# Kernel optimization log

Measured on AMD Instinct MI355X. Metric: run time of the kernel, lower is better.

## Reference

```python
import jax, jax.numpy as jnp
import numpy as np

BN_EPS = 1e-5


def setup_inputs() -> dict:
    key = jax.random.key(0)
    k1, k2, k3 = jax.random.split(key, 3)
    N, C_IN, C_OUT, K = 200000, 32, 64, 27
    data_in = jax.random.normal(k1, (1, C_IN, N, 1), dtype=jnp.float32)
    # Octree neighbor table: for each octant, indices of its 27 (3x3x3) neighbors.
    # ocnn uses -1 for empty neighbors; indices here are all valid, but the
    # reference still masks negatives for faithfulness.
    neigh = jax.random.randint(k2, (N, K), 0, N, dtype=jnp.int64)
    weight = jax.random.normal(k3, (C_OUT, C_IN, K), dtype=jnp.float32) * 0.05
    bn_gamma = jnp.ones((C_OUT,), dtype=jnp.float32)
    bn_beta = jnp.zeros((C_OUT,), dtype=jnp.float32)
    return {"data_in": data_in, "neigh": neigh, "weight": weight,
            "bn_gamma": bn_gamma, "bn_beta": bn_beta}


def reference(data_in, neigh, weight, bn_gamma, bn_beta):
    # data_in: [1, C_in, N, 1] (ocnn octree feature layout)
    x = data_in[0, :, :, 0]                      # [C_in, N]
    valid = neigh >= 0                           # [N, 27]
    idx = jnp.where(valid, neigh, 0)
    # octree2col: gather 27 neighbor features per octant -> [C_in, N, 27]
    col = x[:, idx] * valid[None, :, :].astype(x.dtype)
    # grouped GEMM: weight [C_out, C_in, 27] contracted with col
    out = jnp.einsum('ock,cnk->on', weight, col)  # [C_out, N]
    # BatchNorm2d in training mode: batch stats over the node axis, biased var
    mean = jnp.mean(out, axis=1, keepdims=True)
    var = jnp.mean(jnp.square(out - mean), axis=1, keepdims=True)
    out = (out - mean) * jax.lax.rsqrt(var + BN_EPS)
    out = out * bn_gamma[:, None] + bn_beta[:, None]
    out = jax.nn.relu(out)
    return out[None, :, :, None]                 # [1, C_out, N, 1]
```

## Files before the change

kernel.cpp:

```cpp
#include <hip/hip_runtime.h>

#define N_PTS 200000
#define C_IN  32
#define C_OUT 64
#define K_NB  27
#define BN_EPS 1e-5f
#define CBLK  3125

using bf16x8 = __attribute__((ext_vector_type(8))) short;
using f32x4  = __attribute__((ext_vector_type(4))) float;

typedef const __attribute__((address_space(1))) char GP;
typedef __attribute__((address_space(3))) char LP;

#define M_WT_OFF  0
#define M_AB_OFF  114688
#define M_PS_OFF  131072
#define M_XT_OFF  2097152
#define M_RAW_OFF 14897216
#define M_WS_NEED_B ((size_t)M_XT_OFF + (size_t)(N_PTS + 1) * C_IN * 2)
#define M_WS_NEED_A ((size_t)M_RAW_OFF + (size_t)C_OUT * N_PTS * 2)

#define F_WTK_OFF 0
#define F_AB_OFF  221184
#define F_PS_OFF  221824

__device__ __forceinline__ unsigned short f2bf(float f) {
    unsigned int u = __float_as_uint(f);
    u = (u + 0x7fffu + ((u >> 16) & 1u)) >> 16;
    return (unsigned short)u;
}
__device__ __forceinline__ unsigned short f2h(float f) {
    _Float16 h = (_Float16)f;
    unsigned short u; __builtin_memcpy(&u, &h, 2); return u;
}
__device__ __forceinline__ float h2f(unsigned short u) {
    _Float16 h; __builtin_memcpy(&h, &u, 2); return (float)h;
}

__global__ void k_prep(const float* __restrict__ x, const float* __restrict__ w,
                       unsigned short* __restrict__ xt, unsigned short* __restrict__ wt) {
    if (blockIdx.x < 782) {
        int n = blockIdx.x * 256 + threadIdx.x;
        if (n > N_PTS) return;
        unsigned short row[C_IN];
        if (n == N_PTS) {
#pragma unroll
            for (int c = 0; c < C_IN; ++c) row[c] = 0;
        } else {
#pragma unroll
            for (int c = 0; c < C_IN; ++c) row[c] = f2bf(x[(long long)c * N_PTS + n]);
        }
        uint4* dst = (uint4*)(xt + (long long)n * C_IN);
#pragma unroll
        for (int q = 0; q < 4; ++q) dst[q] = ((const uint4*)row)[q];
    } else {
        int i = (blockIdx.x - 782) * 256 + threadIdx.x;
        if (i >= 28 * C_OUT * C_IN) return;
        int c = i & 31, o = (i >> 5) & 63, k = i >> 11;
        wt[i] = (k < K_NB) ? f2bf(w[(o * C_IN + c) * K_NB + k]) : (unsigned short)0;
    }
}

template <int RAW16>
__launch_bounds__(256, 5)
__global__ void k_conv_mfma(const unsigned short* __restrict__ xt,
                            const int* __restrict__ neigh,
                            const unsigned short* __restrict__ wt,
                            float* __restrict__ out,
                            unsigned short* __restrict__ raw16,
                            float* __restrict__ ps) {
    __shared__ __align__(16) char lds_raw[6 * 4096 + K_NB * 64 * 4];
    char* bufB = lds_raw;
    int*  ntb  = (int*)(lds_raw + 24576);

    const int lane = threadIdx.x & 63;
    const int w    = threadIdx.x >> 6;
    const int l15  = lane & 15, lq = lane >> 4;
    const int n0   = blockIdx.x * 64;

    {
        int p  = threadIdx.x & 63;
        int kb = (threadIdx.x >> 6) * 7;
        const int* nrow = neigh + (long long)(n0 + p) * K_NB;
#pragma unroll
        for (int i = 0; i < 7; ++i) {
            int kk = kb + i;
            if (kk < K_NB) {
                int t = nrow[kk];
                ntb[kk * 64 + p] = ((unsigned)t < N_PTS) ? t : N_PTS;
            }
        }
    }
    __syncthreads();

    const char* xtb = (const char*)xt;
    const unsigned short* wtA = wt + w * 512 + l15 * 32 + lq * 8;
    const unsigned qoff = (unsigned)(lq * 16);

    unsigned bufB_a = (unsigned)(unsigned long long)(LP*)lds_raw;
    unsigned ntb_a  = bufB_a + 24576;
    unsigned badr   = bufB_a + (unsigned)(lq * 256 + l15 * 16);
    unsigned tadr   = ntb_a + (unsigned)(w * 64 + l15 * 4);

    f32x4 acc0 = {0.f,0.f,0.f,0.f}, acc1 = {0.f,0.f,0.f,0.f},
          acc2 = {0.f,0.f,0.f,0.f}, acc3 = {0.f,0.f,0.f,0.f};
    bf16x8 Ar[4];
    int tcur;

#define PSTEP(KK) \
    asm volatile("ds_read_b32 %0, %1 offset:%2" : "=v"(tcur) : "v"(tadr), "i"((KK)*256)); \
    asm volatile("s_waitcnt lgkmcnt(0)" ::: "memory"); \
    __builtin_amdgcn_sched_barrier(0); \
    __builtin_amdgcn_global_load_lds((GP*)(xtb + (unsigned long long)(unsigned)tcur * 64ull + qoff), \
        (LP*)(bufB + (KK)*4096 + w*1024), 16, 0, 0); \
    asm volatile("global_load_dwordx4 %0, %1, off" : "=v"(Ar[(KK)&3]) : "v"(wtA + (KK)*2048)); \
    __builtin_amdgcn_sched_barrier(0);

    PSTEP(0) PSTEP(1) PSTEP(2) PSTEP(3)
#undef PSTEP
    asm volatile("ds_read_b32 %0, %1 offset:%2" : "=v"(tcur) : "v"(tadr), "i"(4*256));

#define STEP(K, VM, PF, NT, LG) { \
    if (PF) { \
        asm volatile("s_waitcnt lgkmcnt(0)" ::: "memory"); \
        __builtin_amdgcn_sched_barrier(0); \
        __builtin_amdgcn_global_load_lds((GP*)(xtb + (unsigned long long)(unsigned)tcur * 64ull + qoff), \
            (LP*)(bufB + (((K)+4)%6)*4096 + w*1024), 16, 0, 0); \
    } \
    __builtin_amdgcn_sched_barrier(0); \
    asm volatile("s_waitcnt vmcnt(%0)" :: "i"(VM) : "memory"); \
    __builtin_amdgcn_sched_barrier(0); \
    asm volatile("s_barrier" ::: "memory"); \
    __builtin_amdgcn_sched_barrier(0); \
    bf16x8 b0, b1, b2, b3; \
    asm volatile("ds_read_b128 %0, %1 offset:%2" : "=v"(b0) : "v"(badr), "i"(((K)%6)*4096 + 0)); \
    asm volatile("ds_read_b128 %0, %1 offset:%2" : "=v"(b1) : "v"(badr), "i"(((K)%6)*4096 + 1024)); \
    asm volatile("ds_read_b128 %0, %1 offset:%2" : "=v"(b2) : "v"(badr), "i"(((K)%6)*4096 + 2048)); \
    asm volatile("ds_read_b128 %0, %1 offset:%2" : "=v"(b3) : "v"(badr), "i"(((K)%6)*4096 + 3072)); \
    if (NT) { asm volatile("ds_read_b32 %0, %1 offset:%2" : "=v"(tcur) : "v"(tadr), "i"(((K)+5)*256)); } \
    asm volatile("s_waitcnt lgkmcnt(%0)" :: "i"(LG) : "memory"); \
    __builtin_amdgcn_sched_barrier(0); \
    acc0 = __builtin_amdgcn_mfma_f32_16x16x32_bf16(Ar[(K)&3], b0, acc0, 0, 0, 0); \
    acc1 = __builtin_amdgcn_mfma_f32_16x16x32_bf16(Ar[(K)&3], b1, acc1, 0, 0, 0); \
    acc2 = __builtin_amdgcn_mfma_f32_16x16x32_bf16(Ar[(K)&3], b2, acc2, 0, 0, 0); \
    acc3 = __builtin_amdgcn_mfma_f32_16x16x32_bf16(Ar[(K)&3], b3, acc3, 0, 0, 0); \
    if (PF) { \
        asm volatile("global_load_dwordx4 %0, %1, off" : "=v"(Ar[((K)+4)&3]) : "v"(wtA + ((K)+4)*2048)); \
    } \
    __builtin_amdgcn_sched_barrier(0); \
}

    STEP(0,7,1,1,1)  STEP(1,7,1,1,1)  STEP(2,7,1,1,1)  STEP(3,7,1,1,1)
    STEP(4,7,1,1,1)  STEP(5,7,1,1,1)  STEP(6,7,1,1,1)  STEP(7,7,1,1,1)
    STEP(8,7,1,1,1)  STEP(9,7,1,1,1)  STEP(10,7,1,1,1) STEP(11,7,1,1,1)
    STEP(12,7,1,1,1) STEP(13,7,1,1,1) STEP(14,7,1,1,1) STEP(15,7,1,1,1)
    STEP(16,7,1,1,1) STEP(17,7,1,1,1) STEP(18,7,1,1,1) STEP(19,7,1,1,1)
    STEP(20,7,1,1,1) STEP(21,7,1,1,1) STEP(22,7,1,0,0)
    STEP(23,6,0,0,0) STEP(24,4,0,0,0) STEP(25,2,0,0,0) STEP(26,0,0,0,0)
#undef STEP

    asm volatile("s_waitcnt vmcnt(0) lgkmcnt(0)" ::: "memory");
    __builtin_amdgcn_sched_barrier(0);

    if (RAW16) {
#pragma unroll
        for (int r = 0; r < 4; ++r) {
            unsigned short* o = raw16 + (long long)(16 * w + lq * 4 + r) * N_PTS + n0 + l15;
            o[0]  = f2h(acc0[r]);
            o[16] = f2h(acc1[r]);
            o[32] = f2h(acc2[r]);
            o[48] = f2h(acc3[r]);
        }
    } else {
#pragma unroll
        for (int r = 0; r < 4; ++r) {
            float* o = out + (long long)(16 * w + lq * 4 + r) * N_PTS + n0 + l15;
            o[0]  = acc0[r];
            o[16] = acc1[r];
            o[32] = acc2[r];
            o[48] = acc3[r];
        }
    }

    f32x4 s  = acc0 + acc1 + acc2 + acc3;
    f32x4 sq = acc0 * acc0 + acc1 * acc1 + acc2 * acc2 + acc3 * acc3;
#pragma unroll
    for (int d = 1; d < 16; d <<= 1) {
#pragma unroll
        for (int r = 0; r < 4; ++r) {
            s[r]  += __shfl_xor(s[r], d);
            sq[r] += __shfl_xor(sq[r], d);
        }
    }
    if (l15 == 0) {
#pragma unroll
        for (int r = 0; r < 4; ++r) {
            int ch = 16 * w + lq * 4 + r;
            ps[blockIdx.x * 128 + ch]      = s[r];
            ps[blockIdx.x * 128 + 64 + ch] = sq[r];
        }
    }
}

__global__ void k_stats2(const float* __restrict__ ps, const float* __restrict__ gamma,
                         const float* __restrict__ beta, float* __restrict__ ab) {
    int ch = blockIdx.x;
    float s = 0.f, s2 = 0.f;
    for (int b = threadIdx.x; b < CBLK; b += 256) {
        s  += ps[b * 128 + ch];
        s2 += ps[b * 128 + 64 + ch];
    }
#pragma unroll
    for (int off = 32; off > 0; off >>= 1) {
        s  += __shfl_down(s, off, 64);
        s2 += __shfl_down(s2, off, 64);
    }
    __shared__ float r0[4], r1[4];
    int wv = threadIdx.x >> 6;
    if ((threadIdx.x & 63) == 0) { r0[wv] = s; r1[wv] = s2; }
    __syncthreads();
    if (threadIdx.x == 0) {
        float S  = r0[0] + r0[1] + r0[2] + r0[3];
        float S2 = r1[0] + r1[1] + r1[2] + r1[3];
        float mean = S / (float)N_PTS;
        float var  = S2 / (float)N_PTS - mean * mean;
        float a = gamma[ch] * rsqrtf(var + BN_EPS);
        float b = beta[ch] - mean * a;
        ab[ch]      = a;
        ab[64 + ch] = b;
    }
}

__global__ void k_norm16(const unsigned short* __restrict__ raw16, float* __restrict__ out,
                         const float* __restrict__ ab) {
    int i = blockIdx.x * 256 + threadIdx.x;
    const int tot8 = (C_OUT * N_PTS) / 8;
    if (i >= tot8) return;
    int o = (int)(((long long)i * 8) / N_PTS);
    float a = ab[o], b = ab[64 + o];
    union { uint4 u4; unsigned short us[8]; } U;
    U.u4 = ((const uint4*)raw16)[i];
    float4 r0, r1;
    r0.x = fmaxf(fmaf(h2f(U.us[0]), a, b), 0.f);
    r0.y = fmaxf(fmaf(h2f(U.us[1]), a, b), 0.f);
    r0.z = fmaxf(fmaf(h2f(U.us[2]), a, b), 0.f);
    r0.w = fmaxf(fmaf(h2f(U.us[3]), a, b), 0.f);
    r1.x = fmaxf(fmaf(h2f(U.us[4]), a, b), 0.f);
    r1.y = fmaxf(fmaf(h2f(U.us[5]), a, b), 0.f);
    r1.z = fmaxf(fmaf(h2f(U.us[6]), a, b), 0.f);
    r1.w = fmaxf(fmaf(h2f(U.us[7]), a, b), 0.f);
    ((float4*)out)[2 * i]     = r0;
    ((float4*)out)[2 * i + 1] = r1;
}

__global__ void k_norm(float* __restrict__ out, const float* __restrict__ ab) {
    int i = blockIdx.x * 256 + threadIdx.x;
    const int total4 = (C_OUT * N_PTS) / 4;
    if (i >= total4) return;
    int o = (i * 4) / N_PTS;
    float a = ab[o], b = ab[64 + o];
    float4 v = ((float4*)out)[i];
    v.x = fmaxf(fmaf(v.x, a, b), 0.f);
    v.y = fmaxf(fmaf(v.y, a, b), 0.f);
    v.z = fmaxf(fmaf(v.z, a, b), 0.f);
    v.w = fmaxf(fmaf(v.w, a, b), 0.f);
    ((float4*)out)[i] = v;
}

__global__ void k_wt_f32(const float* __restrict__ w, float* __restrict__ wtk) {
    int i = blockIdx.x * 256 + threadIdx.x;
    if (i >= K_NB * C_IN * C_OUT) return;
    int o = i & 63, r = i >> 6, c = r & 31, k = r >> 5;
    wtk[i] = w[(o * C_IN + c) * K_NB + k];
}

__launch_bounds__(256, 1)
__global__ void k_conv_f32(const float* __restrict__ src, const int* __restrict__ neigh,
                           const float* __restrict__ wtk, float* __restrict__ out) {
    __shared__ float wt_s[C_IN * C_OUT];
    const int lane = threadIdx.x & 63;
    const int wave = threadIdx.x >> 6;
    const int n0   = blockIdx.x * 64 + wave * 16;
    float acc[16];
#pragma unroll
    for (int p = 0; p < 16; ++p) acc[p] = 0.f;
    for (int k = 0; k < K_NB; ++k) {
        __syncthreads();
#pragma unroll
        for (int j = 0; j < 8; ++j)
            wt_s[threadIdx.x + j * 256] = wtk[k * (C_IN * C_OUT) + threadIdx.x + j * 256];
        __syncthreads();
        int t[16];
#pragma unroll
        for (int p = 0; p < 16; ++p) t[p] = neigh[(n0 + p) * K_NB + k];
#pragma unroll
        for (int c = 0; c < C_IN; ++c) {
            float wv = wt_s[c * C_OUT + lane];
#pragma unroll
            for (int p = 0; p < 16; ++p) {
                float xv = (t[p] >= 0) ? src[(long long)c * N_PTS + t[p]] : 0.f;
                acc[p] = fmaf(wv, xv, acc[p]);
            }
        }
    }
    float4* dst = (float4*)(out + (long long)lane * N_PTS + n0);
#pragma unroll
    for (int q = 0; q < 4; ++q) dst[q] = ((const float4*)acc)[q];
}

__global__ void k_stats1(const float* __restrict__ raw, float* __restrict__ ps) {
    int o = blockIdx.x & 63, sl = blockIdx.x >> 6;
    const int per = N_PTS / 8;
    const float4* row = (const float4*)(raw + (long long)o * N_PTS + (long long)sl * per);
    float s = 0.f, s2 = 0.f;
    for (int i = threadIdx.x; i < per / 4; i += 256) {
        float4 v = row[i];
        s  += v.x + v.y + v.z + v.w;
        s2 += v.x * v.x + v.y * v.y + v.z * v.z + v.w * v.w;
    }
#pragma unroll
    for (int off = 32; off > 0; off >>= 1) {
        s  += __shfl_down(s, off, 64);
        s2 += __shfl_down(s2, off, 64);
    }
    __shared__ float r0[4], r1[4];
    int wv = threadIdx.x >> 6;
    if ((threadIdx.x & 63) == 0) { r0[wv] = s; r1[wv] = s2; }
    __syncthreads();
    if (threadIdx.x == 0) {
        ps[blockIdx.x]       = r0[0] + r0[1] + r0[2] + r0[3];
        ps[512 + blockIdx.x] = r1[0] + r1[1] + r1[2] + r1[3];
    }
}

__global__ void k_stats2f(const float* __restrict__ ps, const float* __restrict__ gamma,
                          const float* __restrict__ beta, float* __restrict__ ab) {
    int o = threadIdx.x;
    float S = 0.f, S2 = 0.f;
#pragma unroll
    for (int sl = 0; sl < 8; ++sl) {
        S  += ps[sl * 64 + o];
        S2 += ps[512 + sl * 64 + o];
    }
    float mean = S / (float)N_PTS;
    float var  = S2 / (float)N_PTS - mean * mean;
    float a = gamma[o] * rsqrtf(var + BN_EPS);
    float b = beta[o] - mean * a;
    ab[o]      = a;
    ab[64 + o] = b;
}

extern "C" void kernel_launch(void* const* d_in, const int* in_sizes, int n_in,
                              void* d_out, int out_size, void* d_ws, size_t ws_size,
                              hipStream_t stream) {
    const float* x   = (const float*)d_in[0];
    const int*   nb  = (const int*)d_in[1];
    const float* w   = (const float*)d_in[2];
    const float* gam = (const float*)d_in[3];
    const float* bet = (const float*)d_in[4];
    float* out = (float*)d_out;
    char* ws = (char*)d_ws;

    if (ws_size >= M_WS_NEED_B) {
        unsigned short* wt  = (unsigned short*)(ws + M_WT_OFF);
        float*          ab  = (float*)(ws + M_AB_OFF);
        float*          ps  = (float*)(ws + M_PS_OFF);
        unsigned short* xt  = (unsigned short*)(ws + M_XT_OFF);
        unsigned short* r16 = (unsigned short*)(ws + M_RAW_OFF);

        k_prep<<<1006, 256, 0, stream>>>(x, w, xt, wt);
        if (ws_size >= M_WS_NEED_A) {
            k_conv_mfma<1><<<CBLK, 256, 0, stream>>>(xt, nb, wt, out, r16, ps);
            k_stats2<<<C_OUT, 256, 0, stream>>>(ps, gam, bet, ab);
            k_norm16<<<(C_OUT * N_PTS / 8 + 255) / 256, 256, 0, stream>>>(r16, out, ab);
        } else {
            k_conv_mfma<0><<<CBLK, 256, 0, stream>>>(xt, nb, wt, out, r16, ps);
            k_stats2<<<C_OUT, 256, 0, stream>>>(ps, gam, bet, ab);
            k_norm<<<((C_OUT * N_PTS) / 4 + 255) / 256, 256, 0, stream>>>(out, ab);
        }
    } else {
        float* wtk  = (float*)(ws + F_WTK_OFF);
        float* ab   = (float*)(ws + F_AB_OFF);
        float* ps   = (float*)(ws + F_PS_OFF);
        k_wt_f32<<<(K_NB * C_IN * C_OUT + 255) / 256, 256, 0, stream>>>(w, wtk);
        k_conv_f32<<<N_PTS / 64, 256, 0, stream>>>(x, nb, wtk, out);
        k_stats1<<<512, 256, 0, stream>>>(out, ps);
        k_stats2f<<<1, 64, 0, stream>>>(ps, gam, bet, ab);
        k_norm<<<((C_OUT * N_PTS) / 4 + 255) / 256, 256, 0, stream>>>(out, ab);
    }
}
```

Measured before the change: 123.4 us.

## Fuse conv, BN stats and normalize into one cooperative persistent kernel

Replaces the conv, stats and normalize kernel chain with a single cooperative kernel. Each of 1280 blocks processes up to three 64-point chunks and keeps fp16-packed results in registers. Channel sums are accumulated with global atomics, and after a grid-wide sync each block normalizes and writes its outputs directly. This removes the fp16 raw intermediate round trip through memory and two launches, at the cost of a grid sync, atomic contention and higher register pressure. It keeps the old path as a fallback if the cooperative launch fails.

```diff
diff --git a/kernel.cpp b/kernel.cpp
--- a/kernel.cpp
+++ b/kernel.cpp
@@ -1,4 +1,5 @@
 #include <hip/hip_runtime.h>
+#include <hip/hip_cooperative_groups.h>
 
 #define N_PTS 200000
 #define C_IN  32
@@ -6,6 +7,7 @@
 #define K_NB  27
 #define BN_EPS 1e-5f
 #define CBLK  3125
+#define FGRID 1280
 
 using bf16x8 = __attribute__((ext_vector_type(8))) short;
 using f32x4  = __attribute__((ext_vector_type(4))) float;
@@ -62,23 +64,11 @@
     }
 }
 
-template <int RAW16>
-__launch_bounds__(256, 5)
-__global__ void k_conv_mfma(const unsigned short* __restrict__ xt,
-                            const int* __restrict__ neigh,
-                            const unsigned short* __restrict__ wt,
-                            float* __restrict__ out,
-                            unsigned short* __restrict__ raw16,
-                            float* __restrict__ ps) {
-    __shared__ __align__(16) char lds_raw[6 * 4096 + K_NB * 64 * 4];
-    char* bufB = lds_raw;
-    int*  ntb  = (int*)(lds_raw + 24576);
-
-    const int lane = threadIdx.x & 63;
-    const int w    = threadIdx.x >> 6;
-    const int l15  = lane & 15, lq = lane >> 4;
-    const int n0   = blockIdx.x * 64;
-
+__device__ __forceinline__ void conv_chunk(int n0, const char* xtb,
+                                           const int* __restrict__ neigh,
+                                           const unsigned short* wtA, unsigned qoff,
+                                           unsigned badr, unsigned tadr,
+                                           char* bufB, int* ntb, int w, f32x4 acc[4]) {
     {
         int p  = threadIdx.x & 63;
         int kb = (threadIdx.x >> 6) * 7;
@@ -94,17 +84,8 @@
     }
     __syncthreads();
 
-    const char* xtb = (const char*)xt;
-    const unsigned short* wtA = wt + w * 512 + l15 * 32 + lq * 8;
-    const unsigned qoff = (unsigned)(lq * 16);
-
-    unsigned bufB_a = (unsigned)(unsigned long long)(LP*)lds_raw;
-    unsigned ntb_a  = bufB_a + 24576;
-    unsigned badr   = bufB_a + (unsigned)(lq * 256 + l15 * 16);
-    unsigned tadr   = ntb_a + (unsigned)(w * 64 + l15 * 4);
-
-    f32x4 acc0 = {0.f,0.f,0.f,0.f}, acc1 = {0.f,0.f,0.f,0.f},
-          acc2 = {0.f,0.f,0.f,0.f}, acc3 = {0.f,0.f,0.f,0.f};
+    acc[0] = f32x4{0.f,0.f,0.f,0.f}; acc[1] = f32x4{0.f,0.f,0.f,0.f};
+    acc[2] = f32x4{0.f,0.f,0.f,0.f}; acc[3] = f32x4{0.f,0.f,0.f,0.f};
     bf16x8 Ar[4];
     int tcur;
 
@@ -141,10 +122,10 @@
     if (NT) { asm volatile("ds_read_b32 %0, %1 offset:%2" : "=v"(tcur) : "v"(tadr), "i"(((K)+5)*256)); } \
     asm volatile("s_waitcnt lgkmcnt(%0)" :: "i"(LG) : "memory"); \
     __builtin_amdgcn_sched_barrier(0); \
-    acc0 = __builtin_amdgcn_mfma_f32_16x16x32_bf16(Ar[(K)&3], b0, acc0, 0, 0, 0); \
-    acc1 = __builtin_amdgcn_mfma_f32_16x16x32_bf16(Ar[(K)&3], b1, acc1, 0, 0, 0); \
-    acc2 = __builtin_amdgcn_mfma_f32_16x16x32_bf16(Ar[(K)&3], b2, acc2, 0, 0, 0); \
-    acc3 = __builtin_amdgcn_mfma_f32_16x16x32_bf16(Ar[(K)&3], b3, acc3, 0, 0, 0); \
+    acc[0] = __builtin_amdgcn_mfma_f32_16x16x32_bf16(Ar[(K)&3], b0, acc[0], 0, 0, 0); \
+    acc[1] = __builtin_amdgcn_mfma_f32_16x16x32_bf16(Ar[(K)&3], b1, acc[1], 0, 0, 0); \
+    acc[2] = __builtin_amdgcn_mfma_f32_16x16x32_bf16(Ar[(K)&3], b2, acc[2], 0, 0, 0); \
+    acc[3] = __builtin_amdgcn_mfma_f32_16x16x32_bf16(Ar[(K)&3], b3, acc[3], 0, 0, 0); \
     if (PF) { \
         asm volatile("global_load_dwordx4 %0, %1, off" : "=v"(Ar[((K)+4)&3]) : "v"(wtA + ((K)+4)*2048)); \
     } \
@@ -162,29 +143,160 @@
 
     asm volatile("s_waitcnt vmcnt(0) lgkmcnt(0)" ::: "memory");
     __builtin_amdgcn_sched_barrier(0);
+}
+
+__launch_bounds__(256, 5)
+__global__ void k_fused(const unsigned short* __restrict__ xt,
+                        const int* __restrict__ neigh,
+                        const unsigned short* __restrict__ wt,
+                        const float* __restrict__ gam,
+                        const float* __restrict__ bet,
+                        float* __restrict__ out,
+                        float* __restrict__ sums) {
+    __shared__ __align__(16) char lds_raw[6 * 4096 + K_NB * 64 * 4];
+    char* bufB = lds_raw;
+    int*  ntb  = (int*)(lds_raw + 24576);
+
+    const int lane = threadIdx.x & 63;
+    const int w    = threadIdx.x >> 6;
+    const int l15  = lane & 15, lq = lane >> 4;
+
+    const char* xtb = (const char*)xt;
+    const unsigned short* wtA = wt + w * 512 + l15 * 32 + lq * 8;
+    const unsigned qoff = (unsigned)(lq * 16);
+    unsigned bufB_a = (unsigned)(unsigned long long)(LP*)lds_raw;
+    unsigned ntb_a  = bufB_a + 24576;
+    unsigned badr   = bufB_a + (unsigned)(lq * 256 + l15 * 16);
+    unsigned tadr   = ntb_a + (unsigned)(w * 64 + l15 * 4);
+
+    const int c0 = blockIdx.x;
+    const int c1 = blockIdx.x + FGRID;
+    const int c2 = blockIdx.x + 2 * FGRID;
+    const bool has2 = (c2 < CBLK);
+
+    f32x4 acc[4];
+    f32x4 sr  = {0.f,0.f,0.f,0.f};
+    f32x4 sqr = {0.f,0.f,0.f,0.f};
+    unsigned pk0[8], pk1[8], pk2[8];
+
+#define EPILOG(PK) { \
+    f32x4 s_ = acc[0] + acc[1] + acc[2] + acc[3]; \
+    f32x4 q_ = acc[0]*acc[0] + acc[1]*acc[1] + acc[2]*acc[2] + acc[3]*acc[3]; \
+    _Pragma("unroll") \
+    for (int d_ = 1; d_ < 16; d_ <<= 1) { \
+        _Pragma("unroll") \
+        for (int r_ = 0; r_ < 4; ++r_) { \
+            s_[r_] += __shfl_xor(s_[r_], d_); \
+            q_[r_] += __shfl_xor(q_[r_], d_); \
+        } \
+    } \
+    sr += s_; sqr += q_; \
+    _Pragma("unroll") \
+    for (int g_ = 0; g_ < 4; ++g_) { \
+        PK[2*g_]   = (unsigned)f2h(acc[g_][0]) | ((unsigned)f2h(acc[g_][1]) << 16); \
+        PK[2*g_+1] = (unsigned)f2h(acc[g_][2]) | ((unsigned)f2h(acc[g_][3]) << 16); \
+    } \
+}
+
+    conv_chunk(c0 * 64, xtb, neigh, wtA, qoff, badr, tadr, bufB, ntb, w, acc);
+    EPILOG(pk0)
+    conv_chunk(c1 * 64, xtb, neigh, wtA, qoff, badr, tadr, bufB, ntb, w, acc);
+    EPILOG(pk1)
+    if (has2) {
+        conv_chunk(c2 * 64, xtb, neigh, wtA, qoff, badr, tadr, bufB, ntb, w, acc);
+        EPILOG(pk2)
+    }
+#undef EPILOG
+
+    if (l15 == 0) {
+#pragma unroll
+        for (int r = 0; r < 4; ++r) {
+            int ch = 16 * w + lq * 4 + r;
+            atomicAdd(&sums[ch],      sr[r]);
+            atomicAdd(&sums[64 + ch], sqr[r]);
+        }
+    }
+    __threadfence();
+    cooperative_groups::this_grid().sync();
+
+    float a_[4], b_[4];
+#pragma unroll
+    for (int r = 0; r < 4; ++r) {
+        int ch = 16 * w + lq * 4 + r;
+        float S  = sums[ch];
+        float S2 = sums[64 + ch];
+        float mean = S / (float)N_PTS;
+        float var  = S2 / (float)N_PTS - mean * mean;
+        a_[r] = gam[ch] * rsqrtf(var + BN_EPS);
+        b_[r] = bet[ch] - mean * a_[r];
+    }
+
+#define WRITEC(CID, PK) { \
+    _Pragma("unroll") \
+    for (int r_ = 0; r_ < 4; ++r_) { \
+        float* o_ = out + (long long)(16 * w + lq * 4 + r_) * N_PTS + (CID) * 64 + l15; \
+        _Pragma("unroll") \
+        for (int g_ = 0; g_ < 4; ++g_) { \
+            unsigned short h_ = (unsigned short)(PK[2*g_ + (r_ >> 1)] >> (16 * (r_ & 1))); \
+            o_[16 * g_] = fmaxf(fmaf(h2f(h_), a_[r_], b_[r_]), 0.f); \
+        } \
+    } \
+}
+    WRITEC(c0, pk0)
+    WRITEC(c1, pk1)
+    if (has2) { WRITEC(c2, pk2) }
+#undef WRITEC
+}
+
+template <int RAW16>
+__launch_bounds__(256, 5)
+__global__ void k_conv_mfma(const unsigned short* __restrict__ xt,
+                            const int* __restrict__ neigh,
+                            const unsigned short* __restrict__ wt,
+                            float* __restrict__ out,
+                            unsigned short* __restrict__ raw16,
+                            float* __restrict__ ps) {
+    __shared__ __align__(16) char lds_raw[6 * 4096 + K_NB * 64 * 4];
+    char* bufB = lds_raw;
+    int*  ntb  = (int*)(lds_raw + 24576);
+    const int lane = threadIdx.x & 63;
+    const int w    = threadIdx.x >> 6;
+    const int l15  = lane & 15, lq = lane >> 4;
+    const int n0   = blockIdx.x * 64;
+
+    const char* xtb = (const char*)xt;
+    const unsigned short* wtA = wt + w * 512 + l15 * 32 + lq * 8;
+    const unsigned qoff = (unsigned)(lq * 16);
+    unsigned bufB_a = (unsigned)(unsigned long long)(LP*)lds_raw;
+    unsigned ntb_a  = bufB_a + 24576;
+    unsigned badr   = bufB_a + (unsigned)(lq * 256 + l15 * 16);
+    unsigned tadr   = ntb_a + (unsigned)(w * 64 + l15 * 4);
+
+    f32x4 acc[4];
+    conv_chunk(n0, xtb, neigh, wtA, qoff, badr, tadr, bufB, ntb, w, acc);
 
     if (RAW16) {
 #pragma unroll
         for (int r = 0; r < 4; ++r) {
             unsigned short* o = raw16 + (long long)(16 * w + lq * 4 + r) * N_PTS + n0 + l15;
-            o[0]  = f2h(acc0[r]);
-            o[16] = f2h(acc1[r]);
-            o[32] = f2h(acc2[r]);
-            o[48] = f2h(acc3[r]);
+            o[0]  = f2h(acc[0][r]);
+            o[16] = f2h(acc[1][r]);
+            o[32] = f2h(acc[2][r]);
+            o[48] = f2h(acc[3][r]);
         }
     } else {
 #pragma unroll
         for (int r = 0; r < 4; ++r) {
             float* o = out + (long long)(16 * w + lq * 4 + r) * N_PTS + n0 + l15;
-            o[0]  = acc0[r];
-            o[16] = acc1[r];
-            o[32] = acc2[r];
-            o[48] = acc3[r];
-        }
-    }
-
-    f32x4 s  = acc0 + acc1 + acc2 + acc3;
-    f32x4 sq = acc0 * acc0 + acc1 * acc1 + acc2 * acc2 + acc3 * acc3;
+            o[0]  = acc[0][r];
+            o[16] = acc[1][r];
+            o[32] = acc[2][r];
+            o[48] = acc[3][r];
+        }
+    }
+
+    f32x4 s  = acc[0] + acc[1] + acc[2] + acc[3];
+    f32x4 sq = acc[0]*acc[0] + acc[1]*acc[1] + acc[2]*acc[2] + acc[3]*acc[3];
 #pragma unroll
     for (int d = 1; d < 16; d <<= 1) {
 #pragma unroll
@@ -363,21 +475,31 @@
     char* ws = (char*)d_ws;
 
     if (ws_size >= M_WS_NEED_B) {
-        unsigned short* wt  = (unsigned short*)(ws + M_WT_OFF);
-        float*          ab  = (float*)(ws + M_AB_OFF);
-        float*          ps  = (float*)(ws + M_PS_OFF);
-        unsigned short* xt  = (unsigned short*)(ws + M_XT_OFF);
-        unsigned short* r16 = (unsigned short*)(ws + M_RAW_OFF);
+        unsigned short* wt   = (unsigned short*)(ws + M_WT_OFF);
+        float*          sums = (float*)(ws + M_AB_OFF);
+        float*          ps   = (float*)(ws + M_PS_OFF);
+        unsigned short* xt   = (unsigned short*)(ws + M_XT_OFF);
+        unsigned short* r16  = (unsigned short*)(ws + M_RAW_OFF);
 
         k_prep<<<1006, 256, 0, stream>>>(x, w, xt, wt);
-        if (ws_size >= M_WS_NEED_A) {
-            k_conv_mfma<1><<<CBLK, 256, 0, stream>>>(xt, nb, wt, out, r16, ps);
-            k_stats2<<<C_OUT, 256, 0, stream>>>(ps, gam, bet, ab);
-            k_norm16<<<(C_OUT * N_PTS / 8 + 255) / 256, 256, 0, stream>>>(r16, out, ab);
-        } else {
-            k_conv_mfma<0><<<CBLK, 256, 0, stream>>>(xt, nb, wt, out, r16, ps);
-            k_stats2<<<C_OUT, 256, 0, stream>>>(ps, gam, bet, ab);
-            k_norm<<<((C_OUT * N_PTS) / 4 + 255) / 256, 256, 0, stream>>>(out, ab);
+        hipMemsetAsync(sums, 0, 128 * sizeof(float), stream);
+
+        void* kargs[7];
+        kargs[0] = (void*)&xt;  kargs[1] = (void*)&nb;  kargs[2] = (void*)&wt;
+        kargs[3] = (void*)&gam; kargs[4] = (void*)&bet; kargs[5] = (void*)&out;
+        kargs[6] = (void*)&sums;
+        hipError_t ce = hipLaunchCooperativeKernel((const void*)k_fused,
+                                                   dim3(FGRID), dim3(256), kargs, 0, stream);
+        if (ce != hipSuccess) {
+            if (ws_size >= M_WS_NEED_A) {
+                k_conv_mfma<1><<<CBLK, 256, 0, stream>>>(xt, nb, wt, out, r16, ps);
+                k_stats2<<<C_OUT, 256, 0, stream>>>(ps, gam, bet, sums);
+                k_norm16<<<(C_OUT * N_PTS / 8 + 255) / 256, 256, 0, stream>>>(r16, out, sums);
+            } else {
+                k_conv_mfma<0><<<CBLK, 256, 0, stream>>>(xt, nb, wt, out, r16, ps);
+                k_stats2<<<C_OUT, 256, 0, stream>>>(ps, gam, bet, sums);
+                k_norm<<<((C_OUT * N_PTS) / 4 + 255) / 256, 256, 0, stream>>>(out, sums);
+            }
         }
     } else {
         float* wtk  = (float*)(ws + F_WTK_OFF);
```

After: 447.7 us. 263% more time.
